# Optimization experiments

Measured on AMD Instinct MI355X. Metric: run time of the kernel, lower is better.

Reference implementation:

```python
import jax, jax.numpy as jnp
import numpy as np

B, F_BINS, K = 8192, 2048, 6
LS, LBW, BWMAX = 0.1, 0.05, 4.0   # lambda_sparse, lambda_bw_excess, bw_soft_max
LAP, LPK, LUM = 0.5, 0.3, 0.1     # lambda_ap, lambda_peaks, lambda_unmatched
BIG = 1e9


def _huber_mean(p, t):
    # F.huber_loss with delta=1.0, mean reduction
    e = p - t
    a = jnp.abs(e)
    return jnp.mean(jnp.where(a < 1.0, 0.5 * e * e, a - 0.5))


def _soft_match_peaks(pred_cfs, gt_cfs, gt_mask):
    """Greedy nearest-neighbour matching, sequential over the K GT slots."""
    b, k = pred_cfs.shape
    dist = jnp.abs(gt_cfs[:, :, None] - pred_cfs[:, None, :])  # [B, K_gt, K_pred]
    active = gt_mask > 0.5                                      # [B, K]

    def step(slot_used, inp):
        d_j, act_j = inp                               # [B, K], [B]
        d_m = jnp.where(slot_used, BIG, d_j)
        best = jnp.argmin(d_m, axis=1)                 # [B]
        idx = jnp.where(act_j, best, -1)
        hit = (best[:, None] == jnp.arange(k)[None, :]) & act_j[:, None]
        return slot_used | hit, idx

    used0 = jnp.zeros((b, k), dtype=bool)
    used, match_idx = jax.lax.scan(step, used0, (jnp.moveaxis(dist, 1, 0), active.T))
    matched = used.astype(pred_cfs.dtype)
    return match_idx.T, matched, 1.0 - matched  # [B,K] long, [B,K] float, [B,K] float


def _total_loss(pred_psd, true_psd, cfs, amps, bws, exponent, offset,
                gt_cfs, gt_amps, gt_bws, gt_offset, gt_exponent, peak_mask):
    # reconstruction terms
    l_recon = _huber_mean(pred_psd, true_psd)
    l_sparse = jnp.mean(amps)
    bw_excess = jnp.maximum(bws - BWMAX, 0.0)
    l_bw = jnp.mean(bw_excess * bw_excess)
    total = l_recon + LS * l_sparse + LBW * l_bw

    # supervised aperiodic term
    l_ap = jnp.mean((exponent[:, 0] - gt_exponent) ** 2) + jnp.mean((offset[:, 0] - gt_offset) ** 2)

    # matched peak terms
    match_idx, matched, unmatched = _soft_match_peaks(cfs, gt_cfs, peak_mask)
    n_real = jnp.maximum(jnp.sum(peak_mask), 1.0)
    idx = jnp.maximum(match_idx, 0)
    # torch leaves GT columns with no active entry at zero
    col_any = jnp.any(peak_mask > 0.5, axis=0)

    def gathered(v):
        return jnp.where(col_any[None, :], jnp.take_along_axis(v, idx, axis=1), 0.0)

    def masked_mse(p, t):
        return jnp.sum(((p - t) ** 2) * peak_mask) / n_real

    l_peaks = (masked_mse(gathered(cfs), gt_cfs)
               + masked_mse(gathered(amps), gt_amps)
               + masked_mse(gathered(bws), gt_bws))
    l_um = jnp.sum(amps * unmatched) / jnp.maximum(jnp.sum(unmatched), 1.0)

    return total + LAP * l_ap + LPK * l_peaks + LUM * l_um


def setup_inputs() -> dict:
    key = jax.random.key(0)
    ks = jax.random.split(key, 13)
    peak_mask = jax.random.randint(ks[7], (B, K), 0, 2).astype(jnp.float32)
    return {
        "pred_psd": jax.random.normal(ks[0], (B, F_BINS), dtype=jnp.float32),
        "true_psd": jax.random.normal(ks[1], (B, F_BINS), dtype=jnp.float32),
        "cfs": jax.random.uniform(ks[2], (B, K), minval=1.0, maxval=30.0),
        "amps": jax.random.uniform(ks[3], (B, K), minval=0.0, maxval=1.5),
        "bws": jax.random.uniform(ks[4], (B, K), minval=0.5, maxval=6.0),
        "exponent": jax.random.normal(ks[5], (B, 1), dtype=jnp.float32),
        "offset": jax.random.normal(ks[6], (B, 1), dtype=jnp.float32),
        # GT peaks: sorted ascending, zero-padded where mask==0
        "gt_cfs": jnp.sort(jax.random.uniform(ks[8], (B, K), minval=1.0, maxval=30.0), axis=1) * peak_mask,
        "gt_amps": jax.random.uniform(ks[9], (B, K), minval=0.0, maxval=1.5) * peak_mask,
        "gt_bws": jax.random.uniform(ks[10], (B, K), minval=0.5, maxval=6.0) * peak_mask,
        "gt_offset": jax.random.normal(ks[11], (B,), dtype=jnp.float32),
        "gt_exponent": jax.random.normal(ks[12], (B,), dtype=jnp.float32),
        "peak_mask": peak_mask,
    }


def reference(pred_psd, true_psd, cfs, amps, bws, exponent, offset,
              gt_cfs, gt_amps, gt_bws, gt_offset, gt_exponent, peak_mask):
    return _total_loss(pred_psd, true_psd, cfs, amps, bws, exponent, offset,
                       gt_cfs, gt_amps, gt_bws, gt_offset, gt_exponent, peak_mask)
```

## Files before the change

kernel.cpp:

```cpp
#include <hip/hip_runtime.h>

#define BATCH   8192
#define FBINS   2048
#define KSLOTS  6

#define HTHREADS 512
#define HWAVES   8
#define HBLOCKS  512
#define TILES    8
#define TILE_F4  1024
#define WTILE_F4 (TILE_F4 / HWAVES)
#define BLK_F4   (TILES * TILE_F4)

#define RBLOCKS   (BATCH / HTHREADS)
#define TOTBLOCKS (HBLOCKS + RBLOCKS)

#define LS   0.1f
#define LBW  0.05f
#define BWMAX 4.0f
#define LAP  0.5f
#define LPK  0.3f
#define LUM  0.1f

__device__ __forceinline__ void gload16(const float4* g, float4* l) {
    __builtin_amdgcn_global_load_lds(
        (const __attribute__((address_space(1))) void*)g,
        (__attribute__((address_space(3))) void*)l, 16, 0, 0);
}

__device__ __forceinline__ float huber4(float4 a, float4 b) {
    float s = 0.f;
    { float e = a.x - b.x; float ab = fabsf(e); s += (ab < 1.f) ? 0.5f * e * e : ab - 0.5f; }
    { float e = a.y - b.y; float ab = fabsf(e); s += (ab < 1.f) ? 0.5f * e * e : ab - 0.5f; }
    { float e = a.z - b.z; float ab = fabsf(e); s += (ab < 1.f) ? 0.5f * e * e : ab - 0.5f; }
    { float e = a.w - b.w; float ab = fabsf(e); s += (ab < 1.f) ? 0.5f * e * e : ab - 0.5f; }
    return s;
}

__global__ __launch_bounds__(HTHREADS) void fused_partial(
    const float* __restrict__ pred,  const float* __restrict__ tgt,
    const float* __restrict__ cfs,   const float* __restrict__ amps,
    const float* __restrict__ bws,   const float* __restrict__ expn,
    const float* __restrict__ offs,  const float* __restrict__ gt_cfs,
    const float* __restrict__ gt_amps, const float* __restrict__ gt_bws,
    const float* __restrict__ gt_off, const float* __restrict__ gt_exp,
    const float* __restrict__ mask,
    float* __restrict__ hpart, float* __restrict__ rpart)
{
    __shared__ float4 ldsA[2][TILE_F4];
    __shared__ float4 ldsB[2][TILE_F4];
    __shared__ float  wred[HWAVES][8];

    const int tid  = threadIdx.x;
    const int wave = tid >> 6;
    const int lane = tid & 63;

    if (blockIdx.x < HBLOCKS) {
        const float4* __restrict__ a4 = (const float4*)pred;
        const float4* __restrict__ b4 = (const float4*)tgt;
        const int woff  = wave * WTILE_F4;
        const int gbase = blockIdx.x * BLK_F4 + woff + lane;

        {
            const float4* ga = a4 + gbase;
            const float4* gb = b4 + gbase;
            gload16(ga,      &ldsA[0][woff]);
            gload16(ga + 64, &ldsA[0][woff + 64]);
            gload16(gb,      &ldsB[0][woff]);
            gload16(gb + 64, &ldsB[0][woff + 64]);
        }

        float ssum = 0.f;
        #pragma unroll
        for (int t = 0; t < TILES; t++) {
            const int buf = t & 1;
            if (t + 1 < TILES) {
                const float4* ga = a4 + gbase + (t + 1) * TILE_F4;
                const float4* gb = b4 + gbase + (t + 1) * TILE_F4;
                gload16(ga,      &ldsA[buf ^ 1][woff]);
                gload16(ga + 64, &ldsA[buf ^ 1][woff + 64]);
                gload16(gb,      &ldsB[buf ^ 1][woff]);
                gload16(gb + 64, &ldsB[buf ^ 1][woff + 64]);
                asm volatile("s_waitcnt vmcnt(4)" ::: "memory");
            } else {
                asm volatile("s_waitcnt vmcnt(0)" ::: "memory");
            }
            __builtin_amdgcn_sched_barrier(0);

            float4 a0 = ldsA[buf][woff + lane];
            float4 b0 = ldsB[buf][woff + lane];
            float4 a1 = ldsA[buf][woff + 64 + lane];
            float4 b1 = ldsB[buf][woff + 64 + lane];
            ssum += huber4(a0, b0);
            ssum += huber4(a1, b1);
        }

        #pragma unroll
        for (int o = 32; o > 0; o >>= 1)
            ssum += __shfl_down(ssum, o, 64);
        if (lane == 0) wred[wave][0] = ssum;
        __syncthreads();
        if (tid == 0) {
            float t = 0.f;
            #pragma unroll
            for (int w = 0; w < HWAVES; w++) t += wred[w][0];
            hpart[blockIdx.x] = t;
        }
        return;
    }

    const int rb = blockIdx.x - HBLOCKS;
    const int b = rb * HTHREADS + tid;

    float acc[7];
    #pragma unroll
    for (int c = 0; c < 7; c++) acc[c] = 0.f;

    {
        float c[KSLOTS], a[KSLOTS], w[KSLOTS];
        float gc[KSLOTS], ga[KSLOTS], gw[KSLOTS], m[KSLOTS];
        #pragma unroll
        for (int i = 0; i < KSLOTS; i++) {
            c[i]  = cfs[b * KSLOTS + i];
            a[i]  = amps[b * KSLOTS + i];
            w[i]  = bws[b * KSLOTS + i];
            gc[i] = gt_cfs[b * KSLOTS + i];
            ga[i] = gt_amps[b * KSLOTS + i];
            gw[i] = gt_bws[b * KSLOTS + i];
            m[i]  = mask[b * KSLOTS + i];
        }

        bool used[KSLOTS];
        #pragma unroll
        for (int i = 0; i < KSLOTS; i++) used[i] = false;

        for (int j = 0; j < KSLOTS; j++) {
            if (m[j] > 0.5f) {
                int best = -1;
                float bd = 3.402823e+38f;
                #pragma unroll
                for (int i = 0; i < KSLOTS; i++) {
                    if (!used[i]) {
                        float d = fabsf(gc[j] - c[i]);
                        if (d < bd) { bd = d; best = i; }
                    }
                }
                used[best] = true;
                float dc = c[best] - gc[j];
                float da = a[best] - ga[j];
                float dw = w[best] - gw[j];
                acc[3] += dc * dc + da * da + dw * dw;
                acc[4] += 1.f;
            }
        }

        #pragma unroll
        for (int i = 0; i < KSLOTS; i++) {
            acc[0] += a[i];
            float ex = fmaxf(w[i] - BWMAX, 0.f);
            acc[1] += ex * ex;
            if (!used[i]) { acc[5] += 1.f; acc[6] += a[i]; }
        }

        float de = expn[b] - gt_exp[b];
        float dof = offs[b] - gt_off[b];
        acc[2] = de * de + dof * dof;
    }

    #pragma unroll
    for (int c = 0; c < 7; c++) {
        float v = acc[c];
        #pragma unroll
        for (int o = 32; o > 0; o >>= 1)
            v += __shfl_down(v, o, 64);
        acc[c] = v;
    }
    if (lane == 0) {
        #pragma unroll
        for (int c = 0; c < 7; c++) wred[wave][c] = acc[c];
    }
    __syncthreads();
    if (tid < 7) {
        float t = 0.f;
        #pragma unroll
        for (int w = 0; w < HWAVES; w++) t += wred[w][tid];
        rpart[7 * rb + tid] = t;
    }
}

__global__ __launch_bounds__(256) void finalize(
    const float* __restrict__ hpart, const float* __restrict__ rpart,
    float* __restrict__ out)
{
    __shared__ double sm[256];
    double s = 0.0;
    #pragma unroll
    for (int r = 0; r < HBLOCKS / 256; r++)
        s += (double)hpart[r * 256 + threadIdx.x];
    sm[threadIdx.x] = s;
    __syncthreads();
    for (int o = 128; o > 0; o >>= 1) {
        if (threadIdx.x < o) sm[threadIdx.x] += sm[threadIdx.x + o];
        __syncthreads();
    }

    if (threadIdx.x == 0) {
        double huber_total = sm[0];
        double acc[7];
        for (int c = 0; c < 7; c++) acc[c] = 0.0;
        for (int blk = 0; blk < RBLOCKS; blk++)
            for (int c = 0; c < 7; c++)
                acc[c] += (double)rpart[7 * blk + c];

        double l_recon  = huber_total / ((double)BATCH * FBINS);
        double l_sparse = acc[0] / ((double)BATCH * KSLOTS);
        double l_bw     = acc[1] / ((double)BATCH * KSLOTS);
        double l_ap     = acc[2] / (double)BATCH;
        double n_real   = acc[4] > 1.0 ? acc[4] : 1.0;
        double l_peaks  = acc[3] / n_real;
        double n_um     = acc[5] > 1.0 ? acc[5] : 1.0;
        double l_um     = acc[6] / n_um;

        double total = l_recon + (double)LS * l_sparse + (double)LBW * l_bw
                     + (double)LAP * l_ap + (double)LPK * l_peaks + (double)LUM * l_um;
        out[0] = (float)total;
    }
}

extern "C" void kernel_launch(void* const* d_in, const int* in_sizes, int n_in,
                              void* d_out, int out_size, void* d_ws, size_t ws_size,
                              hipStream_t stream) {
    const float* pred_psd = (const float*)d_in[0];
    const float* true_psd = (const float*)d_in[1];
    const float* cfs      = (const float*)d_in[2];
    const float* amps     = (const float*)d_in[3];
    const float* bws      = (const float*)d_in[4];
    const float* expn     = (const float*)d_in[5];
    const float* offs     = (const float*)d_in[6];
    const float* gt_cfs   = (const float*)d_in[7];
    const float* gt_amps  = (const float*)d_in[8];
    const float* gt_bws   = (const float*)d_in[9];
    const float* gt_off   = (const float*)d_in[10];
    const float* gt_exp   = (const float*)d_in[11];
    const float* mask     = (const float*)d_in[12];
    float* out = (float*)d_out;

    float* hpart = (float*)d_ws;
    float* rpart = hpart + HBLOCKS;

    fused_partial<<<TOTBLOCKS, HTHREADS, 0, stream>>>(
        pred_psd, true_psd, cfs, amps, bws, expn, offs,
        gt_cfs, gt_amps, gt_bws, gt_off, gt_exp, mask, hpart, rpart);
    finalize<<<1, 256, 0, stream>>>(hpart, rpart, out);
}
```

Baseline: 30.75 us.

## Fuse finalize into main kernel via atomics and last-block reduction

Removes the separate finalize kernel launch. Each block now adds its partial sums into double-precision global accumulators with atomics, and a completion counter lets the last block compute the final loss. The Huber tiles are halved and the block count doubled, so each block does one float4 per lane per tile. This adds a memset launch and contention on the atomics, and it relies on the relaxed atomic ordering being enough for correctness.

```diff
diff --git a/kernel.cpp b/kernel.cpp
--- a/kernel.cpp
+++ b/kernel.cpp
@@ -6,9 +6,9 @@
 
 #define HTHREADS 512
 #define HWAVES   8
-#define HBLOCKS  512
+#define HBLOCKS  1024
 #define TILES    8
-#define TILE_F4  1024
+#define TILE_F4  512
 #define WTILE_F4 (TILE_F4 / HWAVES)
 #define BLK_F4   (TILES * TILE_F4)
 
@@ -37,7 +37,7 @@
     return s;
 }
 
-__global__ __launch_bounds__(HTHREADS) void fused_partial(
+__global__ __launch_bounds__(HTHREADS) void fused_all(
     const float* __restrict__ pred,  const float* __restrict__ tgt,
     const float* __restrict__ cfs,   const float* __restrict__ amps,
     const float* __restrict__ bws,   const float* __restrict__ expn,
@@ -45,7 +45,8 @@
     const float* __restrict__ gt_amps, const float* __restrict__ gt_bws,
     const float* __restrict__ gt_off, const float* __restrict__ gt_exp,
     const float* __restrict__ mask,
-    float* __restrict__ hpart, float* __restrict__ rpart)
+    double* __restrict__ accs, unsigned int* __restrict__ counter,
+    float* __restrict__ out)
 {
     __shared__ float4 ldsA[2][TILE_F4];
     __shared__ float4 ldsB[2][TILE_F4];
@@ -61,38 +62,25 @@
         const int woff  = wave * WTILE_F4;
         const int gbase = blockIdx.x * BLK_F4 + woff + lane;
 
-        {
-            const float4* ga = a4 + gbase;
-            const float4* gb = b4 + gbase;
-            gload16(ga,      &ldsA[0][woff]);
-            gload16(ga + 64, &ldsA[0][woff + 64]);
-            gload16(gb,      &ldsB[0][woff]);
-            gload16(gb + 64, &ldsB[0][woff + 64]);
-        }
+        gload16(a4 + gbase, &ldsA[0][woff]);
+        gload16(b4 + gbase, &ldsB[0][woff]);
 
         float ssum = 0.f;
         #pragma unroll
         for (int t = 0; t < TILES; t++) {
             const int buf = t & 1;
             if (t + 1 < TILES) {
-                const float4* ga = a4 + gbase + (t + 1) * TILE_F4;
-                const float4* gb = b4 + gbase + (t + 1) * TILE_F4;
-                gload16(ga,      &ldsA[buf ^ 1][woff]);
-                gload16(ga + 64, &ldsA[buf ^ 1][woff + 64]);
-                gload16(gb,      &ldsB[buf ^ 1][woff]);
-                gload16(gb + 64, &ldsB[buf ^ 1][woff + 64]);
-                asm volatile("s_waitcnt vmcnt(4)" ::: "memory");
+                gload16(a4 + gbase + (t + 1) * TILE_F4, &ldsA[buf ^ 1][woff]);
+                gload16(b4 + gbase + (t + 1) * TILE_F4, &ldsB[buf ^ 1][woff]);
+                asm volatile("s_waitcnt vmcnt(2)" ::: "memory");
             } else {
                 asm volatile("s_waitcnt vmcnt(0)" ::: "memory");
             }
             __builtin_amdgcn_sched_barrier(0);
 
-            float4 a0 = ldsA[buf][woff + lane];
-            float4 b0 = ldsB[buf][woff + lane];
-            float4 a1 = ldsA[buf][woff + 64 + lane];
-            float4 b1 = ldsB[buf][woff + 64 + lane];
-            ssum += huber4(a0, b0);
-            ssum += huber4(a1, b1);
+            float4 a = ldsA[buf][woff + lane];
+            float4 b = ldsB[buf][woff + lane];
+            ssum += huber4(a, b);
         }
 
         #pragma unroll
@@ -104,126 +92,113 @@
             float t = 0.f;
             #pragma unroll
             for (int w = 0; w < HWAVES; w++) t += wred[w][0];
-            hpart[blockIdx.x] = t;
-        }
-        return;
+            __hip_atomic_fetch_add(&accs[0], (double)t,
+                                   __ATOMIC_RELAXED, __HIP_MEMORY_SCOPE_AGENT);
+        }
+    } else {
+        const int rb = blockIdx.x - HBLOCKS;
+        const int b = rb * HTHREADS + tid;
+
+        float acc[7];
+        #pragma unroll
+        for (int c = 0; c < 7; c++) acc[c] = 0.f;
+
+        {
+            float c[KSLOTS], a[KSLOTS], w[KSLOTS];
+            float gc[KSLOTS], ga[KSLOTS], gw[KSLOTS], m[KSLOTS];
+            #pragma unroll
+            for (int i = 0; i < KSLOTS; i++) {
+                c[i]  = cfs[b * KSLOTS + i];
+                a[i]  = amps[b * KSLOTS + i];
+                w[i]  = bws[b * KSLOTS + i];
+                gc[i] = gt_cfs[b * KSLOTS + i];
+                ga[i] = gt_amps[b * KSLOTS + i];
+                gw[i] = gt_bws[b * KSLOTS + i];
+                m[i]  = mask[b * KSLOTS + i];
+            }
+
+            bool used[KSLOTS];
+            #pragma unroll
+            for (int i = 0; i < KSLOTS; i++) used[i] = false;
+
+            for (int j = 0; j < KSLOTS; j++) {
+                if (m[j] > 0.5f) {
+                    int best = -1;
+                    float bd = 3.402823e+38f;
+                    #pragma unroll
+                    for (int i = 0; i < KSLOTS; i++) {
+                        if (!used[i]) {
+                            float d = fabsf(gc[j] - c[i]);
+                            if (d < bd) { bd = d; best = i; }
+                        }
+                    }
+                    used[best] = true;
+                    float dc = c[best] - gc[j];
+                    float da = a[best] - ga[j];
+                    float dw = w[best] - gw[j];
+                    acc[3] += dc * dc + da * da + dw * dw;
+                    acc[4] += 1.f;
+                }
+            }
+
+            #pragma unroll
+            for (int i = 0; i < KSLOTS; i++) {
+                acc[0] += a[i];
+                float ex = fmaxf(w[i] - BWMAX, 0.f);
+                acc[1] += ex * ex;
+                if (!used[i]) { acc[5] += 1.f; acc[6] += a[i]; }
+            }
+
+            float de = expn[b] - gt_exp[b];
+            float dof = offs[b] - gt_off[b];
+            acc[2] = de * de + dof * dof;
+        }
+
+        #pragma unroll
+        for (int c = 0; c < 7; c++) {
+            float v = acc[c];
+            #pragma unroll
+            for (int o = 32; o > 0; o >>= 1)
+                v += __shfl_down(v, o, 64);
+            acc[c] = v;
+        }
+        if (lane == 0) {
+            #pragma unroll
+            for (int c = 0; c < 7; c++) wred[wave][c] = acc[c];
+        }
+        __syncthreads();
+        if (tid < 7) {
+            float t = 0.f;
+            #pragma unroll
+            for (int w = 0; w < HWAVES; w++) t += wred[w][tid];
+            __hip_atomic_fetch_add(&accs[1 + tid], (double)t,
+                                   __ATOMIC_RELAXED, __HIP_MEMORY_SCOPE_AGENT);
+        }
     }
 
-    const int rb = blockIdx.x - HBLOCKS;
-    const int b = rb * HTHREADS + tid;
-
-    float acc[7];
-    #pragma unroll
-    for (int c = 0; c < 7; c++) acc[c] = 0.f;
-
-    {
-        float c[KSLOTS], a[KSLOTS], w[KSLOTS];
-        float gc[KSLOTS], ga[KSLOTS], gw[KSLOTS], m[KSLOTS];
-        #pragma unroll
-        for (int i = 0; i < KSLOTS; i++) {
-            c[i]  = cfs[b * KSLOTS + i];
-            a[i]  = amps[b * KSLOTS + i];
-            w[i]  = bws[b * KSLOTS + i];
-            gc[i] = gt_cfs[b * KSLOTS + i];
-            ga[i] = gt_amps[b * KSLOTS + i];
-            gw[i] = gt_bws[b * KSLOTS + i];
-            m[i]  = mask[b * KSLOTS + i];
-        }
-
-        bool used[KSLOTS];
-        #pragma unroll
-        for (int i = 0; i < KSLOTS; i++) used[i] = false;
-
-        for (int j = 0; j < KSLOTS; j++) {
-            if (m[j] > 0.5f) {
-                int best = -1;
-                float bd = 3.402823e+38f;
-                #pragma unroll
-                for (int i = 0; i < KSLOTS; i++) {
-                    if (!used[i]) {
-                        float d = fabsf(gc[j] - c[i]);
-                        if (d < bd) { bd = d; best = i; }
-                    }
-                }
-                used[best] = true;
-                float dc = c[best] - gc[j];
-                float da = a[best] - ga[j];
-                float dw = w[best] - gw[j];
-                acc[3] += dc * dc + da * da + dw * dw;
-                acc[4] += 1.f;
-            }
-        }
-
-        #pragma unroll
-        for (int i = 0; i < KSLOTS; i++) {
-            acc[0] += a[i];
-            float ex = fmaxf(w[i] - BWMAX, 0.f);
-            acc[1] += ex * ex;
-            if (!used[i]) { acc[5] += 1.f; acc[6] += a[i]; }
-        }
-
-        float de = expn[b] - gt_exp[b];
-        float dof = offs[b] - gt_off[b];
-        acc[2] = de * de + dof * dof;
-    }
-
-    #pragma unroll
-    for (int c = 0; c < 7; c++) {
-        float v = acc[c];
-        #pragma unroll
-        for (int o = 32; o > 0; o >>= 1)
-            v += __shfl_down(v, o, 64);
-        acc[c] = v;
-    }
-    if (lane == 0) {
-        #pragma unroll
-        for (int c = 0; c < 7; c++) wred[wave][c] = acc[c];
-    }
-    __syncthreads();
-    if (tid < 7) {
-        float t = 0.f;
-        #pragma unroll
-        for (int w = 0; w < HWAVES; w++) t += wred[w][tid];
-        rpart[7 * rb + tid] = t;
-    }
-}
-
-__global__ __launch_bounds__(256) void finalize(
-    const float* __restrict__ hpart, const float* __restrict__ rpart,
-    float* __restrict__ out)
-{
-    __shared__ double sm[256];
-    double s = 0.0;
-    #pragma unroll
-    for (int r = 0; r < HBLOCKS / 256; r++)
-        s += (double)hpart[r * 256 + threadIdx.x];
-    sm[threadIdx.x] = s;
-    __syncthreads();
-    for (int o = 128; o > 0; o >>= 1) {
-        if (threadIdx.x < o) sm[threadIdx.x] += sm[threadIdx.x + o];
-        __syncthreads();
-    }
-
-    if (threadIdx.x == 0) {
-        double huber_total = sm[0];
-        double acc[7];
-        for (int c = 0; c < 7; c++) acc[c] = 0.0;
-        for (int blk = 0; blk < RBLOCKS; blk++)
-            for (int c = 0; c < 7; c++)
-                acc[c] += (double)rpart[7 * blk + c];
-
-        double l_recon  = huber_total / ((double)BATCH * FBINS);
-        double l_sparse = acc[0] / ((double)BATCH * KSLOTS);
-        double l_bw     = acc[1] / ((double)BATCH * KSLOTS);
-        double l_ap     = acc[2] / (double)BATCH;
-        double n_real   = acc[4] > 1.0 ? acc[4] : 1.0;
-        double l_peaks  = acc[3] / n_real;
-        double n_um     = acc[5] > 1.0 ? acc[5] : 1.0;
-        double l_um     = acc[6] / n_um;
-
-        double total = l_recon + (double)LS * l_sparse + (double)LBW * l_bw
-                     + (double)LAP * l_ap + (double)LPK * l_peaks + (double)LUM * l_um;
-        out[0] = (float)total;
+    if (tid == 0) {
+        asm volatile("s_waitcnt vmcnt(0)" ::: "memory");
+        unsigned int prev = __hip_atomic_fetch_add(counter, 1u,
+                               __ATOMIC_RELAXED, __HIP_MEMORY_SCOPE_AGENT);
+        if (prev == TOTBLOCKS - 1) {
+            double v[8];
+            #pragma unroll
+            for (int i = 0; i < 8; i++)
+                v[i] = __hip_atomic_load(&accs[i], __ATOMIC_RELAXED,
+                                         __HIP_MEMORY_SCOPE_AGENT);
+            double l_recon  = v[0] / ((double)BATCH * FBINS);
+            double l_sparse = v[1] / ((double)BATCH * KSLOTS);
+            double l_bw     = v[2] / ((double)BATCH * KSLOTS);
+            double l_ap     = v[3] / (double)BATCH;
+            double n_real   = v[5] > 1.0 ? v[5] : 1.0;
+            double l_peaks  = v[4] / n_real;
+            double n_um     = v[6] > 1.0 ? v[6] : 1.0;
+            double l_um     = v[7] / n_um;
+            double total = l_recon + (double)LS * l_sparse + (double)LBW * l_bw
+                         + (double)LAP * l_ap + (double)LPK * l_peaks
+                         + (double)LUM * l_um;
+            out[0] = (float)total;
+        }
     }
 }
 
@@ -245,11 +220,11 @@
     const float* mask     = (const float*)d_in[12];
     float* out = (float*)d_out;
 
-    float* hpart = (float*)d_ws;
-    float* rpart = hpart + HBLOCKS;
-
-    fused_partial<<<TOTBLOCKS, HTHREADS, 0, stream>>>(
+    double* accs = (double*)d_ws;
+    unsigned int* counter = (unsigned int*)((char*)d_ws + 64);
+
+    hipMemsetAsync(d_ws, 0, 128, stream);
+    fused_all<<<TOTBLOCKS, HTHREADS, 0, stream>>>(
         pred_psd, true_psd, cfs, amps, bws, expn, offs,
-        gt_cfs, gt_amps, gt_bws, gt_off, gt_exp, mask, hpart, rpart);
-    finalize<<<1, 256, 0, stream>>>(hpart, rpart, out);
-}
+        gt_cfs, gt_amps, gt_bws, gt_off, gt_exp, mask, accs, counter, out);
+}
```

After: 41.51 us. +35.0%, slower.
